# Kernel optimization log

Measured on AMD Instinct MI355X. Metric: run time of the kernel, lower is better.

The kernel has to match this reference:

```python
import jax, jax.numpy as jnp
import numpy as np

D_IN = 1024
D_OUT = 1024
SEQ = 4096


def setup_inputs() -> dict:
    key = jax.random.key(0)
    kx, kq, kk, kv = jax.random.split(key, 4)
    x = jax.random.normal(kx, (SEQ, D_IN), dtype=jnp.float32)
    # original uses torch.rand (uniform [0,1)) for parameter init
    w_query = jax.random.uniform(kq, (D_IN, D_OUT), dtype=jnp.float32)
    w_key = jax.random.uniform(kk, (D_IN, D_OUT), dtype=jnp.float32)
    w_value = jax.random.uniform(kv, (D_IN, D_OUT), dtype=jnp.float32)
    return {"x": x, "w_query": w_query, "w_key": w_key, "w_value": w_value}


def reference(x, w_query, w_key, w_value):
    # QKV projections: [S, d_in] @ [d_in, d_out] -> [S, d_out]
    queries = x @ w_query
    keys = x @ w_key
    values = x @ w_value
    scale = keys.shape[-1] ** 0.5
    # full attention matrix [S, S]
    attn_scores = jnp.einsum('sd,td->st', queries, keys)
    attn_weights = jax.nn.softmax(attn_scores / scale, axis=-1)
    context_vecs = attn_weights @ values  # [S, d_out]
    return context_vecs
```

## Files before the change

### kernel.cpp

```cpp
#include <hip/hip_runtime.h>
#include <hip/hip_fp16.h>
#include <math.h>

#define SEQ    4096
#define DMODEL 1024

typedef _Float16 half8   __attribute__((ext_vector_type(8)));
typedef _Float16 half4v  __attribute__((ext_vector_type(4)));
typedef float    floatx4 __attribute__((ext_vector_type(4)));

__device__ inline void split_val(float v, _Float16& h, _Float16& l) {
    _Float16 hh = (_Float16)v;
    h = hh;
    l = (_Float16)(v - (float)hh);
}

__global__ __launch_bounds__(256) void prep(const float* __restrict__ x,
                                            const float* __restrict__ wq,
                                            const float* __restrict__ wk,
                                            const float* __restrict__ wv,
                                            _Float16* __restrict__ x_hi,
                                            _Float16* __restrict__ x_lo,
                                            _Float16* __restrict__ wqkT_hi,
                                            _Float16* __restrict__ wqkT_lo,
                                            _Float16* __restrict__ wvT) {
    __shared__ float tile[32][33];
    const int b = blockIdx.x;
    if (b < 3072) {
        const int which = b >> 10;
        const int bb = b & 1023;
        const int c0 = (bb & 31) * 32;
        const int r0 = (bb >> 5) * 32;
        const float* w = (which == 0) ? wq : (which == 1) ? wk : wv;
        const int tx = threadIdx.x & 31, ty = threadIdx.x >> 5;
#pragma unroll
        for (int j = 0; j < 4; ++j)
            tile[ty * 4 + j][tx] = w[(size_t)(r0 + ty * 4 + j) * DMODEL + c0 + tx];
        __syncthreads();
        if (which < 2) {
            _Float16* th = wqkT_hi + (size_t)which * DMODEL * DMODEL;
            _Float16* tl = wqkT_lo + (size_t)which * DMODEL * DMODEL;
#pragma unroll
            for (int j = 0; j < 4; ++j) {
                float v = tile[tx][ty * 4 + j];
                size_t idx = (size_t)(c0 + ty * 4 + j) * DMODEL + r0 + tx;
                _Float16 h, l;
                split_val(v, h, l);
                th[idx] = h;
                tl[idx] = l;
            }
        } else {
#pragma unroll
            for (int j = 0; j < 4; ++j)
                wvT[(size_t)(c0 + ty * 4 + j) * DMODEL + r0 + tx] =
                    (_Float16)tile[tx][ty * 4 + j];
        }
    } else {
        const int t0 = (b - 3072) * 256 + threadIdx.x;
#pragma unroll
        for (int rep = 0; rep < 4; ++rep) {
            const size_t i = (size_t)t0 + (size_t)rep * 262144;
            floatx4 v = *(const floatx4*)(x + 4 * i);
            half4v h, l;
#pragma unroll
            for (int j = 0; j < 4; ++j) {
                _Float16 hh = (_Float16)v[j];
                _Float16 ll = (_Float16)(v[j] - (float)hh);
                h[j] = hh;
                l[j] = ll;
            }
            *(half4v*)(x_hi + 4 * i) = h;
            *(half4v*)(x_lo + 4 * i) = l;
        }
    }
}

__global__ __launch_bounds__(512, 1) void gemm_qkproj_dp(
    const _Float16* __restrict__ Ahi, const _Float16* __restrict__ Alo,
    const _Float16* __restrict__ Bhi, const _Float16* __restrict__ Blo,
    _Float16* __restrict__ Qh, _Float16* __restrict__ Kh) {
    __shared__ _Float16 Ah[3][128][32];
    __shared__ _Float16 Al[3][128][32];
    __shared__ _Float16 Bh[3][256][32];
    __shared__ _Float16 Bl[3][256][32];

    const int tid  = threadIdx.x;
    const int lane = tid & 63;
    const int wid  = tid >> 6;
    const int wm   = (wid >> 2) * 64;
    const int wn   = (wid & 3) * 64;

    const int rowA0 = blockIdx.y * 128;
    const int colB0 = blockIdx.x * 256;

    const int ar  = tid >> 2;
    const int ag  = tid & 3;
    const int ags = ag ^ ((ar >> 1) & 3);
    const char* aHiS = (const char*)(Ahi + (size_t)(rowA0 + ar) * DMODEL) + ags * 16;
    const char* aLoS = (const char*)(Alo + (size_t)(rowA0 + ar) * DMODEL) + ags * 16;
    const char* bHi0 = (const char*)(Bhi + (size_t)(colB0 + ar) * DMODEL) + ags * 16;
    const char* bHi1 = (const char*)(Bhi + (size_t)(colB0 + ar + 128) * DMODEL) + ags * 16;
    const char* bLo0 = (const char*)(Blo + (size_t)(colB0 + ar) * DMODEL) + ags * 16;
    const char* bLo1 = (const char*)(Blo + (size_t)(colB0 + ar + 128) * DMODEL) + ags * 16;

#define STAGE_Q(tt)                                                                  \
    do {                                                                             \
        const int _s = (tt) % 3;                                                     \
        const size_t _ko = (size_t)(tt) * 64;                                        \
        __builtin_amdgcn_global_load_lds(                                            \
            (const __attribute__((address_space(1))) void*)(aHiS + _ko),             \
            (__attribute__((address_space(3))) void*)&Ah[_s][ar][ag * 8], 16, 0, 0); \
        __builtin_amdgcn_global_load_lds(                                            \
            (const __attribute__((address_space(1))) void*)(aLoS + _ko),             \
            (__attribute__((address_space(3))) void*)&Al[_s][ar][ag * 8], 16, 0, 0); \
        __builtin_amdgcn_global_load_lds(                                            \
            (const __attribute__((address_space(1))) void*)(bHi0 + _ko),             \
            (__attribute__((address_space(3))) void*)&Bh[_s][ar][ag * 8], 16, 0, 0); \
        __builtin_amdgcn_global_load_lds(                                            \
            (const __attribute__((address_space(1))) void*)(bHi1 + _ko),             \
            (__attribute__((address_space(3))) void*)&Bh[_s][ar + 128][ag * 8], 16, 0, 0);\
        __builtin_amdgcn_global_load_lds(                                            \
            (const __attribute__((address_space(1))) void*)(bLo0 + _ko),             \
            (__attribute__((address_space(3))) void*)&Bl[_s][ar][ag * 8], 16, 0, 0); \
        __builtin_amdgcn_global_load_lds(                                            \
            (const __attribute__((address_space(1))) void*)(bLo1 + _ko),             \
            (__attribute__((address_space(3))) void*)&Bl[_s][ar + 128][ag * 8], 16, 0, 0);\
    } while (0)

    const int fm = lane & 15;
    const int fq = lane >> 4;
    const int ck = (fq ^ ((fm >> 1) & 3)) * 8;

    floatx4 acc[4][4] = {};

    auto tile_body = [&](int t, bool do_stage) {
        const int s = t % 3;
        half8 avh[4], avl[4], bvh[4], bvl[4];
#pragma unroll
        for (int i = 0; i < 4; ++i) {
            avh[i] = *(const half8*)&Ah[s][wm + i * 16 + fm][ck];
            avl[i] = *(const half8*)&Al[s][wm + i * 16 + fm][ck];
        }
#pragma unroll
        for (int j = 0; j < 4; ++j) {
            bvh[j] = *(const half8*)&Bh[s][wn + j * 16 + fm][ck];
            bvl[j] = *(const half8*)&Bl[s][wn + j * 16 + fm][ck];
        }
        if (do_stage) STAGE_Q(t + 2);
        asm volatile("" ::: "memory");
        __builtin_amdgcn_s_barrier();
        asm volatile("" ::: "memory");
        __builtin_amdgcn_s_setprio(1);
#pragma unroll
        for (int i = 0; i < 4; ++i)
#pragma unroll
            for (int j = 0; j < 4; ++j)
                acc[i][j] = __builtin_amdgcn_mfma_f32_16x16x32_f16(avh[i], bvh[j], acc[i][j], 0, 0, 0);
#pragma unroll
        for (int i = 0; i < 4; ++i)
#pragma unroll
            for (int j = 0; j < 4; ++j)
                acc[i][j] = __builtin_amdgcn_mfma_f32_16x16x32_f16(avh[i], bvl[j], acc[i][j], 0, 0, 0);
#pragma unroll
        for (int i = 0; i < 4; ++i)
#pragma unroll
            for (int j = 0; j < 4; ++j)
                acc[i][j] = __builtin_amdgcn_mfma_f32_16x16x32_f16(avl[i], bvh[j], acc[i][j], 0, 0, 0);
        __builtin_amdgcn_s_setprio(0);
    };

    STAGE_Q(0);
    STAGE_Q(1);
    asm volatile("s_waitcnt vmcnt(6)" ::: "memory");
    __builtin_amdgcn_s_barrier();
    asm volatile("" ::: "memory");

#pragma unroll 1
    for (int t = 0; t < 30; ++t) {
        tile_body(t, true);
        asm volatile("s_waitcnt vmcnt(6)" ::: "memory");
        __builtin_amdgcn_s_barrier();
        asm volatile("" ::: "memory");
    }
    tile_body(30, false);
    asm volatile("s_waitcnt vmcnt(0)" ::: "memory");
    __builtin_amdgcn_s_barrier();
    asm volatile("" ::: "memory");
    tile_body(31, false);
#undef STAGE_Q

    _Float16* dst = Qh;
    int cbase = colB0;
    if (colB0 >= 1024) { dst = Kh; cbase = colB0 - 1024; }

#pragma unroll
    for (int i = 0; i < 4; ++i) {
        const int growb = rowA0 + wm + i * 16 + fq * 4;
#pragma unroll
        for (int j = 0; j < 4; ++j) {
            const int gcol = wn + j * 16 + fm;
#pragma unroll
            for (int r = 0; r < 4; ++r)
                dst[(size_t)(growb + r) * DMODEL + cbase + gcol] =
                    (_Float16)acc[i][j][r];
        }
    }
}

__global__ __launch_bounds__(512, 2) void gemm_score_dp(
    const _Float16* __restrict__ Qh,
    const _Float16* __restrict__ Kh,
    _Float16* __restrict__ Ph, float* __restrict__ Marr, float* __restrict__ Larr,
    float scale) {
    __shared__ _Float16 As[4][256][32];
    __shared__ _Float16 Bs[4][256][32];

    const int tid  = threadIdx.x;
    const int lane = tid & 63;
    const int wid  = tid >> 6;
    const int wm   = (wid >> 2) * 128;
    const int wn   = (wid & 3) * 64;

    const int lin = blockIdx.y * 16 + blockIdx.x;
    const int swz = (lin & 7) * 32 + (lin >> 3);
    const int rowA0 = (swz >> 4) * 256;
    const int colB0 = (swz & 15) * 256;

    const int pr  = tid >> 2;
    const int pg  = tid & 3;
    const int pgs = pg ^ ((pr >> 1) & 3);

    const char* aSrc0 = (const char*)(Qh + (size_t)(rowA0 + pr) * DMODEL) + pgs * 16;
    const char* aSrc1 = (const char*)(Qh + (size_t)(rowA0 + pr + 128) * DMODEL) + pgs * 16;
    const char* bSrc0 = (const char*)(Kh + (size_t)(colB0 + pr) * DMODEL) + pgs * 16;
    const char* bSrc1 = (const char*)(Kh + (size_t)(colB0 + pr + 128) * DMODEL) + pgs * 16;

#define STAGE_A(t)                                                                  \
    do {                                                                            \
        const int _s = (t) & 3;                                                     \
        const size_t _ko = (size_t)(t) * 64;                                        \
        __builtin_amdgcn_global_load_lds(                                           \
            (const __attribute__((address_space(1))) void*)(aSrc0 + _ko),           \
            (__attribute__((address_space(3))) void*)&As[_s][pr][pg * 8], 16, 0, 0);\
        __builtin_amdgcn_global_load_lds(                                           \
            (const __attribute__((address_space(1))) void*)(aSrc1 + _ko),           \
            (__attribute__((address_space(3))) void*)&As[_s][pr + 128][pg * 8], 16, 0, 0);\
    } while (0)

#define STAGE_B(t)                                                                  \
    do {                                                                            \
        const int _s = (t) & 3;                                                     \
        const size_t _ko = (size_t)(t) * 64;                                        \
        __builtin_amdgcn_global_load_lds(                                           \
            (const __attribute__((address_space(1))) void*)(bSrc0 + _ko),           \
            (__attribute__((address_space(3))) void*)&Bs[_s][pr][pg * 8], 16, 0, 0);\
        __builtin_amdgcn_global_load_lds(                                           \
            (const __attribute__((address_space(1))) void*)(bSrc1 + _ko),           \
            (__attribute__((address_space(3))) void*)&Bs[_s][pr + 128][pg * 8], 16, 0, 0);\
    } while (0)

    const int fm = lane & 15;
    const int fq = lane >> 4;
    const int ck = (fq ^ ((fm >> 1) & 3)) * 8;

    floatx4 acc[8][4] = {};

    auto tile_body = [&](int t, bool do_stage) {
        const int s = t & 3;
        half8 av[4], av2[4], bv[4];
#pragma unroll
        for (int i = 0; i < 4; ++i) av[i]  = *(const half8*)&As[s][wm + i * 16 + fm][ck];
#pragma unroll
        for (int i = 0; i < 4; ++i) av2[i] = *(const half8*)&As[s][wm + 64 + i * 16 + fm][ck];
#pragma unroll
        for (int j = 0; j < 4; ++j) bv[j]  = *(const half8*)&Bs[s][wn + j * 16 + fm][ck];
        if (do_stage) { STAGE_A(t + 3); STAGE_B(t + 3); }
        asm volatile("" ::: "memory");
        __builtin_amdgcn_s_barrier();
        asm volatile("" ::: "memory");
        __builtin_amdgcn_s_setprio(1);
#pragma unroll
        for (int i = 0; i < 4; ++i)
#pragma unroll
            for (int j = 0; j < 4; ++j)
                acc[i][j] = __builtin_amdgcn_mfma_f32_16x16x32_f16(av[i], bv[j], acc[i][j], 0, 0, 0);
#pragma unroll
        for (int i = 0; i < 4; ++i)
#pragma unroll
            for (int j = 0; j < 4; ++j)
                acc[i + 4][j] = __builtin_amdgcn_mfma_f32_16x16x32_f16(av2[i], bv[j], acc[i + 4][j], 0, 0, 0);
        __builtin_amdgcn_s_setprio(0);
    };

    STAGE_A(0); STAGE_B(0);
    STAGE_A(1); STAGE_B(1);
    STAGE_A(2); STAGE_B(2);
    asm volatile("s_waitcnt vmcnt(8)" ::: "memory");
    __builtin_amdgcn_s_barrier();
    asm volatile("" ::: "memory");

#pragma unroll 1
    for (int t = 0; t < 29; ++t) {
        tile_body(t, true);
        asm volatile("s_waitcnt vmcnt(8)" ::: "memory");
        __builtin_amdgcn_s_barrier();
        asm volatile("" ::: "memory");
    }
    tile_body(29, false);
    asm volatile("s_waitcnt vmcnt(4)" ::: "memory");
    __builtin_amdgcn_s_barrier();
    asm volatile("" ::: "memory");
    tile_body(30, false);
    asm volatile("s_waitcnt vmcnt(0)" ::: "memory");
    __builtin_amdgcn_s_barrier();
    asm volatile("" ::: "memory");
    tile_body(31, false);
#undef STAGE_A
#undef STAGE_B

    const int tprime = (colB0 + wn) >> 6;
#pragma unroll
    for (int i = 0; i < 8; ++i) {
#pragma unroll
        for (int r = 0; r < 4; ++r) {
            const int grow = rowA0 + wm + i * 16 + fq * 4 + r;
            float s0 = acc[i][0][r] * scale;
            float s1 = acc[i][1][r] * scale;
            float s2 = acc[i][2][r] * scale;
            float s3 = acc[i][3][r] * scale;
            float mx = fmaxf(fmaxf(s0, s1), fmaxf(s2, s3));
            mx = fmaxf(mx, __shfl_xor(mx, 1));
            mx = fmaxf(mx, __shfl_xor(mx, 2));
            mx = fmaxf(mx, __shfl_xor(mx, 4));
            mx = fmaxf(mx, __shfl_xor(mx, 8));
            float p0 = __expf(s0 - mx);
            float p1 = __expf(s1 - mx);
            float p2 = __expf(s2 - mx);
            float p3 = __expf(s3 - mx);
            float sum = p0 + p1 + p2 + p3;
            sum += __shfl_xor(sum, 1);
            sum += __shfl_xor(sum, 2);
            sum += __shfl_xor(sum, 4);
            sum += __shfl_xor(sum, 8);
            _Float16* prow = Ph + (size_t)grow * SEQ + colB0 + wn + fm;
            prow[0]  = (_Float16)p0;
            prow[16] = (_Float16)p1;
            prow[32] = (_Float16)p2;
            prow[48] = (_Float16)p3;
            if (fm == 0) {
                Marr[(size_t)grow * 64 + tprime] = mx;
                Larr[(size_t)grow * 64 + tprime] = sum;
            }
        }
    }
}

__global__ __launch_bounds__(256) void compute_c(const float* __restrict__ Marr,
                                                 const float* __restrict__ Larr,
                                                 _Float16* __restrict__ CarrT) {
    __shared__ float c_s[64][65];
    const int row0 = blockIdx.x * 64;
    const int wv = threadIdx.x >> 6;
    const int ln = threadIdx.x & 63;

#pragma unroll
    for (int k = 0; k < 16; ++k) {
        const int r = wv * 16 + k;
        float mt = Marr[(size_t)(row0 + r) * 64 + ln];
        float lt = Larr[(size_t)(row0 + r) * 64 + ln];
        float m = mt;
#pragma unroll
        for (int off = 32; off > 0; off >>= 1) m = fmaxf(m, __shfl_xor(m, off));
        float e = __expf(mt - m);
        float L = lt * e;
#pragma unroll
        for (int off = 32; off > 0; off >>= 1) L += __shfl_xor(L, off);
        c_s[r][ln] = e / L;
    }
    __syncthreads();

#pragma unroll
    for (int k = 0; k < 16; ++k) {
        const int t = wv * 16 + k;
        CarrT[(size_t)t * SEQ + row0 + ln] = (_Float16)c_s[ln][t];
    }
}

__global__ __launch_bounds__(512, 1) void gemm_pv_dp(
    const _Float16* __restrict__ P,
    const _Float16* __restrict__ VT,
    const _Float16* __restrict__ CarrT,
    float* __restrict__ out) {
    __shared__ _Float16 As[4][128][64];
    __shared__ _Float16 Bs[4][128][64];
    __shared__ _Float16 cT[64][128];

    const int tid  = threadIdx.x;
    const int lane = tid & 63;
    const int wid  = tid >> 6;
    const int wm   = (wid >> 2) * 64;
    const int wn   = (wid & 3) * 32;

    const int rowA0 = blockIdx.y * 128;
    const int colB0 = blockIdx.x * 128;

    {
        int g = tid;
#pragma unroll
        for (int it = 0; it < 2; ++it, g += 512) {
            const int t  = g >> 4;
            const int r8 = (g & 15) * 8;
            *(half8*)&cT[t][r8] =
                *(const half8*)(CarrT + (size_t)t * SEQ + rowA0 + r8);
        }
    }
    __syncthreads();

    const int prow = tid >> 3;
    const int pgr  = tid & 7;
    const int ags  = pgr ^ (prow & 7);
    const char* aSrc0 = (const char*)(P  + (size_t)(rowA0 + prow) * SEQ) + ags * 16;
    const char* aSrc1 = (const char*)(P  + (size_t)(rowA0 + prow + 64) * SEQ) + ags * 16;
    const char* bSrc0 = (const char*)(VT + (size_t)(colB0 + prow) * SEQ) + ags * 16;
    const char* bSrc1 = (const char*)(VT + (size_t)(colB0 + prow + 64) * SEQ) + ags * 16;

#define STAGE_PA(tt)                                                                \
    do {                                                                            \
        const int _s = (tt) & 3;                                                    \
        const size_t _ko = (size_t)(tt) * 128;                                      \
        __builtin_amdgcn_global_load_lds(                                           \
            (const __attribute__((address_space(1))) void*)(aSrc0 + _ko),           \
            (__attribute__((address_space(3))) void*)&As[_s][prow][pgr * 8], 16, 0, 0);\
        __builtin_amdgcn_global_load_lds(                                           \
            (const __attribute__((address_space(1))) void*)(aSrc1 + _ko),           \
            (__attribute__((address_space(3))) void*)&As[_s][prow + 64][pgr * 8], 16, 0, 0);\
    } while (0)

#define STAGE_PB(tt)                                                                \
    do {                                                                            \
        const int _s = (tt) & 3;                                                    \
        const size_t _ko = (size_t)(tt) * 128;                                      \
        __builtin_amdgcn_global_load_lds(                                           \
            (const __attribute__((address_space(1))) void*)(bSrc0 + _ko),           \
            (__attribute__((address_space(3))) void*)&Bs[_s][prow][pgr * 8], 16, 0, 0);\
        __builtin_amdgcn_global_load_lds(                                           \
            (const __attribute__((address_space(1))) void*)(bSrc1 + _ko),           \
            (__attribute__((address_space(3))) void*)&Bs[_s][prow + 64][pgr * 8], 16, 0, 0);\
    } while (0)

    const int fm = lane & 15;
    const int fq = lane >> 4;
    const int ck0 = ((fq    ) ^ (fm & 7)) * 8;
    const int ck1 = ((fq + 4) ^ (fm & 7)) * 8;

    floatx4 acc[4][2] = {};

    auto tile_body = [&](int t, bool do_stage) {
        const int s = t & 3;
        half8 av[4], av2[4], bv[2], bv2[2];
        _Float16 cs[4];
#pragma unroll
        for (int i = 0; i < 4; ++i) {
            av[i]  = *(const half8*)&As[s][wm + i * 16 + fm][ck0];
            av2[i] = *(const half8*)&As[s][wm + i * 16 + fm][ck1];
            cs[i]  = cT[t][wm + i * 16 + fm];
        }
#pragma unroll
        for (int j = 0; j < 2; ++j) {
            bv[j]  = *(const half8*)&Bs[s][wn + j * 16 + fm][ck0];
            bv2[j] = *(const half8*)&Bs[s][wn + j * 16 + fm][ck1];
        }
#pragma unroll
        for (int i = 0; i < 4; ++i)
#pragma unroll
            for (int e = 0; e < 8; ++e) {
                av[i][e]  *= cs[i];
                av2[i][e] *= cs[i];
            }
        if (do_stage) { STAGE_PA(t + 3); STAGE_PB(t + 3); }
        asm volatile("" ::: "memory");
        __builtin_amdgcn_s_barrier();
        asm volatile("" ::: "memory");
        __builtin_amdgcn_s_setprio(1);
#pragma unroll
        for (int i = 0; i < 4; ++i)
#pragma unroll
            for (int j = 0; j < 2; ++j)
                acc[i][j] = __builtin_amdgcn_mfma_f32_16x16x32_f16(av[i], bv[j], acc[i][j], 0, 0, 0);
#pragma unroll
        for (int i = 0; i < 4; ++i)
#pragma unroll
            for (int j = 0; j < 2; ++j)
                acc[i][j] = __builtin_amdgcn_mfma_f32_16x16x32_f16(av2[i], bv2[j], acc[i][j], 0, 0, 0);
        __builtin_amdgcn_s_setprio(0);
    };

    STAGE_PA(0); STAGE_PB(0);
    STAGE_PA(1); STAGE_PB(1);
    STAGE_PA(2); STAGE_PB(2);
    asm volatile("s_waitcnt vmcnt(8)" ::: "memory");
    __builtin_amdgcn_s_barrier();
    asm volatile("" ::: "memory");

#pragma unroll 1
    for (int t = 0; t < 61; ++t) {
        tile_body(t, true);
        asm volatile("s_waitcnt vmcnt(8)" ::: "memory");
        __builtin_amdgcn_s_barrier();
        asm volatile("" ::: "memory");
    }
    tile_body(61, false);
    asm volatile("s_waitcnt vmcnt(4)" ::: "memory");
    __builtin_amdgcn_s_barrier();
    asm volatile("" ::: "memory");
    tile_body(62, false);
    asm volatile("s_waitcnt vmcnt(0)" ::: "memory");
    __builtin_amdgcn_s_barrier();
    asm volatile("" ::: "memory");
    tile_body(63, false);
#undef STAGE_PA
#undef STAGE_PB

#pragma unroll
    for (int i = 0; i < 4; ++i) {
        const int growb = rowA0 + wm + i * 16 + fq * 4;
#pragma unroll
        for (int j = 0; j < 2; ++j) {
            const int gcol = colB0 + wn + j * 16 + fm;
#pragma unroll
            for (int r = 0; r < 4; ++r)
                out[(size_t)(growb + r) * DMODEL + gcol] = acc[i][j][r];
        }
    }
}

template <int OUT_HALF>
__global__ __launch_bounds__(256) void gemm_h16_n64(
    const _Float16* __restrict__ A, int lda,
    const _Float16* __restrict__ B, int ldb,
    float* __restrict__ Cf, _Float16* __restrict__ Ch,
    int N, int K) {
    __shared__ _Float16 Ah[128][32];
    __shared__ _Float16 Bh[64][32];

    const int tid = threadIdx.x;
    const int lane = tid & 63;
    const int w = tid >> 6;
    const int wm = (w >> 1) * 64;
    const int wn = (w & 1) * 32;

    const int rowA0 = blockIdx.y * 128;
    const int colB0 = blockIdx.x * 64;

    const int sr = lane >> 2;
    const int sc = lane & 3;
    const int ra0 = w * 32 + sr;
    const int ra1 = ra0 + 16;
    const int rb0 = w * 16 + sr;
    const int cga0 = sc ^ ((ra0 >> 1) & 3);
    const int cga1 = sc ^ ((ra1 >> 1) & 3);
    const int cgb0 = sc ^ ((rb0 >> 1) & 3);

    const char* gp[3];
    gp[0] = (const char*)(A + (size_t)(rowA0 + ra0) * lda) + cga0 * 16;
    gp[1] = (const char*)(A + (size_t)(rowA0 + ra1) * lda) + cga1 * 16;
    gp[2] = (const char*)(B + (size_t)(colB0 + rb0) * ldb) + cgb0 * 16;

    _Float16* lp[3] = {
        &Ah[w * 32][0], &Ah[w * 32 + 16][0],
        &Bh[w * 16][0],
    };

    const int fm = lane & 15;
    const int fq = lane >> 4;
    const int ck = ((fq ^ ((fm >> 1) & 3)) * 8);

    floatx4 acc[4][2] = {};

    for (int k0 = 0; k0 < K; k0 += 32) {
#pragma unroll
        for (int t = 0; t < 3; ++t)
            __builtin_amdgcn_global_load_lds(
                (const __attribute__((address_space(1))) void*)gp[t],
                (__attribute__((address_space(3))) void*)lp[t], 16, 0, 0);
#pragma unroll
        for (int t = 0; t < 3; ++t) gp[t] += 64;
        __syncthreads();

        half8 av[4], bv[2];
#pragma unroll
        for (int i = 0; i < 4; ++i)
            av[i] = *(const half8*)&Ah[wm + i * 16 + fm][ck];
#pragma unroll
        for (int j = 0; j < 2; ++j)
            bv[j] = *(const half8*)&Bh[wn + j * 16 + fm][ck];
#pragma unroll
        for (int i = 0; i < 4; ++i)
#pragma unroll
            for (int j = 0; j < 2; ++j)
                acc[i][j] = __builtin_amdgcn_mfma_f32_16x16x32_f16(av[i], bv[j], acc[i][j], 0, 0, 0);
        __syncthreads();
    }

#pragma unroll
    for (int i = 0; i < 4; ++i) {
        const int growb = rowA0 + wm + i * 16 + fq * 4;
#pragma unroll
        for (int j = 0; j < 2; ++j) {
            const int gcol = colB0 + wn + j * 16 + fm;
#pragma unroll
            for (int r = 0; r < 4; ++r) {
                float v = acc[i][j][r];
                size_t idx = (size_t)(growb + r) * N + gcol;
                if (OUT_HALF) Ch[idx] = (_Float16)v;
                else          Cf[idx] = v;
            }
        }
    }
}

extern "C" void kernel_launch(void* const* d_in, const int* in_sizes, int n_in,
                              void* d_out, int out_size, void* d_ws, size_t ws_size,
                              hipStream_t stream) {
    const float* x  = (const float*)d_in[0];
    const float* wq = (const float*)d_in[1];
    const float* wk = (const float*)d_in[2];
    const float* wv = (const float*)d_in[3];
    float* out = (float*)d_out;

    char* base = (char*)d_ws;
    const size_t MB = 1u << 20;
    _Float16* P       = (_Float16*)base;
    _Float16* x_hi    = (_Float16*)(base + 0 * MB);
    _Float16* x_lo    = (_Float16*)(base + 8 * MB);
    _Float16* wqkT_hi = (_Float16*)(base + 16 * MB);
    _Float16* wqkT_lo = (_Float16*)(base + 20 * MB);
    _Float16* wvT     = (_Float16*)(base + 24 * MB);
    float*    Marr    = (float*)(base + 32 * MB);
    float*    Larr    = (float*)(base + 33 * MB);
    _Float16* CarrT   = (_Float16*)(base + 34 * MB);
    _Float16* Qh      = (_Float16*)(base + 64 * MB);
    _Float16* Kh      = (_Float16*)(base + 72 * MB);
    _Float16* VT      = (_Float16*)(base + 96 * MB);

    prep<<<4096, 256, 0, stream>>>(x, wq, wk, wv, x_hi, x_lo, wqkT_hi, wqkT_lo, wvT);

    dim3 gqk(2048 / 256, SEQ / 128);
    gemm_qkproj_dp<<<gqk, dim3(512), 0, stream>>>(x_hi, x_lo, wqkT_hi, wqkT_lo,
                                                  Qh, Kh);
    dim3 gvt(SEQ / 64, DMODEL / 128);
    gemm_h16_n64<1><<<gvt, 256, 0, stream>>>(wvT, DMODEL, x_hi, DMODEL,
                                             nullptr, VT, SEQ, DMODEL);

    dim3 gs(SEQ / 256, SEQ / 256);
    gemm_score_dp<<<gs, dim3(512), 0, stream>>>(Qh, Kh, P, Marr, Larr,
                                                1.0f / 32.0f);

    compute_c<<<SEQ / 64, 256, 0, stream>>>(Marr, Larr, CarrT);

    dim3 gpv(DMODEL / 128, SEQ / 128);
    gemm_pv_dp<<<gpv, dim3(512), 0, stream>>>(P, VT, CarrT, out);
}
```

Measured before the change: 252.1 us.

## Shrink score GEMM tile to 256x128 with 3-stage pipeline and higher occupancy

Shrinks the QK^T score kernel's block tile from 256x256 to 256x128 and cuts each wave's sub-tile from 128x64 to 64x64. The LDS pipeline drops from 4 to 3 stages and the launch bound now asks for 4 blocks per CU. This halves accumulator registers and LDS per block so more blocks can be resident and the grid has twice as many blocks. In exchange, each loaded A element feeds fewer MFMAs, so there is more global and LDS traffic per FLOP, and the prefetch depth is shallower.

```diff
diff --git a/kernel.cpp b/kernel.cpp
--- a/kernel.cpp
+++ b/kernel.cpp
@@ -207,37 +207,35 @@
     }
 }
 
-__global__ __launch_bounds__(512, 2) void gemm_score_dp(
+__global__ __launch_bounds__(512, 4) void gemm_score_dp(
     const _Float16* __restrict__ Qh,
     const _Float16* __restrict__ Kh,
     _Float16* __restrict__ Ph, float* __restrict__ Marr, float* __restrict__ Larr,
     float scale) {
-    __shared__ _Float16 As[4][256][32];
-    __shared__ _Float16 Bs[4][256][32];
+    __shared__ _Float16 As[3][256][32];
+    __shared__ _Float16 Bs[3][128][32];
 
     const int tid  = threadIdx.x;
     const int lane = tid & 63;
     const int wid  = tid >> 6;
-    const int wm   = (wid >> 2) * 128;
-    const int wn   = (wid & 3) * 64;
-
-    const int lin = blockIdx.y * 16 + blockIdx.x;
-    const int swz = (lin & 7) * 32 + (lin >> 3);
-    const int rowA0 = (swz >> 4) * 256;
-    const int colB0 = (swz & 15) * 256;
+    const int wm   = (wid >> 1) * 64;
+    const int wn   = (wid & 1) * 64;
+
+    const int lin = blockIdx.y * 32 + blockIdx.x;
+    const int swz = (lin & 7) * 64 + (lin >> 3);
+    const int rowA0 = (swz >> 5) * 256;
+    const int colB0 = (swz & 31) * 128;
 
     const int pr  = tid >> 2;
     const int pg  = tid & 3;
     const int pgs = pg ^ ((pr >> 1) & 3);
-
     const char* aSrc0 = (const char*)(Qh + (size_t)(rowA0 + pr) * DMODEL) + pgs * 16;
     const char* aSrc1 = (const char*)(Qh + (size_t)(rowA0 + pr + 128) * DMODEL) + pgs * 16;
     const char* bSrc0 = (const char*)(Kh + (size_t)(colB0 + pr) * DMODEL) + pgs * 16;
-    const char* bSrc1 = (const char*)(Kh + (size_t)(colB0 + pr + 128) * DMODEL) + pgs * 16;
-
-#define STAGE_A(t)                                                                  \
+
+#define STAGE_S(t)                                                                  \
     do {                                                                            \
-        const int _s = (t) & 3;                                                     \
+        const int _s = (t) % 3;                                                     \
         const size_t _ko = (size_t)(t) * 64;                                        \
         __builtin_amdgcn_global_load_lds(                                           \
             (const __attribute__((address_space(1))) void*)(aSrc0 + _ko),           \
@@ -245,36 +243,25 @@
         __builtin_amdgcn_global_load_lds(                                           \
             (const __attribute__((address_space(1))) void*)(aSrc1 + _ko),           \
             (__attribute__((address_space(3))) void*)&As[_s][pr + 128][pg * 8], 16, 0, 0);\
-    } while (0)
-
-#define STAGE_B(t)                                                                  \
-    do {                                                                            \
-        const int _s = (t) & 3;                                                     \
-        const size_t _ko = (size_t)(t) * 64;                                        \
         __builtin_amdgcn_global_load_lds(                                           \
             (const __attribute__((address_space(1))) void*)(bSrc0 + _ko),           \
             (__attribute__((address_space(3))) void*)&Bs[_s][pr][pg * 8], 16, 0, 0);\
-        __builtin_amdgcn_global_load_lds(                                           \
-            (const __attribute__((address_space(1))) void*)(bSrc1 + _ko),           \
-            (__attribute__((address_space(3))) void*)&Bs[_s][pr + 128][pg * 8], 16, 0, 0);\
     } while (0)
 
     const int fm = lane & 15;
     const int fq = lane >> 4;
     const int ck = (fq ^ ((fm >> 1) & 3)) * 8;
 
-    floatx4 acc[8][4] = {};
+    floatx4 acc[4][4] = {};
 
     auto tile_body = [&](int t, bool do_stage) {
-        const int s = t & 3;
-        half8 av[4], av2[4], bv[4];
-#pragma unroll
-        for (int i = 0; i < 4; ++i) av[i]  = *(const half8*)&As[s][wm + i * 16 + fm][ck];
-#pragma unroll
-        for (int i = 0; i < 4; ++i) av2[i] = *(const half8*)&As[s][wm + 64 + i * 16 + fm][ck];
-#pragma unroll
-        for (int j = 0; j < 4; ++j) bv[j]  = *(const half8*)&Bs[s][wn + j * 16 + fm][ck];
-        if (do_stage) { STAGE_A(t + 3); STAGE_B(t + 3); }
+        const int s = t % 3;
+        half8 av[4], bv[4];
+#pragma unroll
+        for (int i = 0; i < 4; ++i) av[i] = *(const half8*)&As[s][wm + i * 16 + fm][ck];
+#pragma unroll
+        for (int j = 0; j < 4; ++j) bv[j] = *(const half8*)&Bs[s][wn + j * 16 + fm][ck];
+        if (do_stage) STAGE_S(t + 2);
         asm volatile("" ::: "memory");
         __builtin_amdgcn_s_barrier();
         asm volatile("" ::: "memory");
@@ -284,43 +271,32 @@
 #pragma unroll
             for (int j = 0; j < 4; ++j)
                 acc[i][j] = __builtin_amdgcn_mfma_f32_16x16x32_f16(av[i], bv[j], acc[i][j], 0, 0, 0);
-#pragma unroll
-        for (int i = 0; i < 4; ++i)
-#pragma unroll
-            for (int j = 0; j < 4; ++j)
-                acc[i + 4][j] = __builtin_amdgcn_mfma_f32_16x16x32_f16(av2[i], bv[j], acc[i + 4][j], 0, 0, 0);
         __builtin_amdgcn_s_setprio(0);
     };
 
-    STAGE_A(0); STAGE_B(0);
-    STAGE_A(1); STAGE_B(1);
-    STAGE_A(2); STAGE_B(2);
-    asm volatile("s_waitcnt vmcnt(8)" ::: "memory");
+    STAGE_S(0);
+    STAGE_S(1);
+    asm volatile("s_waitcnt vmcnt(3)" ::: "memory");
     __builtin_amdgcn_s_barrier();
     asm volatile("" ::: "memory");
 
 #pragma unroll 1
-    for (int t = 0; t < 29; ++t) {
+    for (int t = 0; t < 30; ++t) {
         tile_body(t, true);
-        asm volatile("s_waitcnt vmcnt(8)" ::: "memory");
+        asm volatile("s_waitcnt vmcnt(3)" ::: "memory");
         __builtin_amdgcn_s_barrier();
         asm volatile("" ::: "memory");
     }
-    tile_body(29, false);
-    asm volatile("s_waitcnt vmcnt(4)" ::: "memory");
-    __builtin_amdgcn_s_barrier();
-    asm volatile("" ::: "memory");
     tile_body(30, false);
     asm volatile("s_waitcnt vmcnt(0)" ::: "memory");
     __builtin_amdgcn_s_barrier();
     asm volatile("" ::: "memory");
     tile_body(31, false);
-#undef STAGE_A
-#undef STAGE_B
+#undef STAGE_S
 
     const int tprime = (colB0 + wn) >> 6;
 #pragma unroll
-    for (int i = 0; i < 8; ++i) {
+    for (int i = 0; i < 4; ++i) {
 #pragma unroll
         for (int r = 0; r < 4; ++r) {
             const int grow = rowA0 + wm + i * 16 + fq * 4 + r;
@@ -652,7 +628,7 @@
     gemm_h16_n64<1><<<gvt, 256, 0, stream>>>(wvT, DMODEL, x_hi, DMODEL,
                                              nullptr, VT, SEQ, DMODEL);
 
-    dim3 gs(SEQ / 256, SEQ / 256);
+    dim3 gs(SEQ / 128, SEQ / 256);
     gemm_score_dp<<<gs, dim3(512), 0, stream>>>(Qh, Kh, P, Marr, Larr,
                                                 1.0f / 32.0f);
 
```

New measurement: 257.4 us. +2.1%, slower.
